# Kernel optimization log

Measured on AMD Instinct MI355X. Metric: run time of the kernel, lower is better.

Reference implementation:

```python
import jax, jax.numpy as jnp
import numpy as np

TEMPERATURE = 0.07
TAU_THRESHOLD = 0.5

B, D, K = 32768, 512, 2048


def _l2_normalize(x, axis=-1, eps=1e-12):
    # matches torch F.normalize: x / max(||x||, eps)
    n = jnp.linalg.norm(x, axis=axis, keepdims=True)
    return x / jnp.maximum(n, eps)


def setup_inputs() -> dict:
    key = jax.random.key(0)
    k1, k2, k3, k4 = jax.random.split(key, 4)
    embeddings = jax.random.normal(k1, (B, D), dtype=jnp.float32)
    best_similarity = jax.random.uniform(k2, (B,), dtype=jnp.float32)
    global_prototypes = jax.random.normal(k3, (K, D), dtype=jnp.float32)
    prototype_confidence = jax.random.uniform(k4, (K,), dtype=jnp.float32)
    return {
        "embeddings": embeddings,
        "best_similarity": best_similarity,
        "global_prototypes": global_prototypes,
        "prototype_confidence": prototype_confidence,
    }


def reference(embeddings, best_similarity, global_prototypes, prototype_confidence):
    en = _l2_normalize(embeddings, axis=1)          # [B, D]
    pn = _l2_normalize(global_prototypes, axis=1)   # [K, D]
    sims = jnp.einsum("bd,kd->bk", en, pn)          # [B, K] cosine sims
    best_proto_idx = jnp.argmax(sims, axis=1)       # [B]

    logits = sims / TEMPERATURE
    log_probs = jax.nn.log_softmax(logits, axis=1)  # [B, K]
    probs = jnp.exp(log_probs)
    entropy = -jnp.sum(probs * log_probs, axis=1)   # [B]
    max_entropy = jnp.log(jnp.float32(K))
    entropy_norm = entropy / (max_entropy + 1e-8)
    tau_adaptive = TAU_THRESHOLD - 0.2 * entropy_norm

    # confidence_weighted gating
    batch_conf = prototype_confidence[best_proto_idx]                     # [B]
    sigmoid_gate = jax.nn.sigmoid((best_similarity - tau_adaptive) / TEMPERATURE)
    gate = batch_conf * sigmoid_gate                                      # [B]

    target_protos = pn[best_proto_idx]                                    # [B, D]
    dist = jnp.linalg.norm(en - target_protos, axis=1)                    # [B]
    L_proto = jnp.mean(gate * dist)
    return (L_proto, gate)
```

## Files before the change

### kernel.cpp

```cpp
#include <hip/hip_runtime.h>
#include <math.h>


#define NB 32768
#define ND 512
#define NK 2048
#define TEMPR 0.07f
#define INV_T 14.285714285714286f
#define DX 5.0e-3f

typedef unsigned short u16;
typedef unsigned long long u64;
using bf16x8 = __attribute__((ext_vector_type(8))) short;
using u16x8 = __attribute__((ext_vector_type(8))) unsigned short;
using f32x16 = __attribute__((ext_vector_type(16))) float;

__device__ inline u16 bf_hi(float x) {
  unsigned u = __float_as_uint(x);
  u = u + 0x7FFFu + ((u >> 16) & 1u);
  return (u16)(u >> 16);
}
__device__ inline float bf_tof(u16 h) {
  return __uint_as_float(((unsigned)h) << 16);
}
__device__ inline void gload_lds16(const void* g, void* l) {
  __builtin_amdgcn_global_load_lds((const __attribute__((address_space(1))) void*)g,
                                   (__attribute__((address_space(3))) void*)l, 16, 0, 0);
}
#define MF(a, b, c) __builtin_amdgcn_mfma_f32_32x32x16_bf16((a), (b), (c), 0, 0, 0)

#define WAIT_LGKM0 { asm volatile("s_waitcnt lgkmcnt(0)" ::: "memory"); \
                     __builtin_amdgcn_sched_barrier(0); }
#define WAIT_VM6   { asm volatile("s_waitcnt vmcnt(6)" ::: "memory"); \
                     __builtin_amdgcn_sched_barrier(0); }
#define SBAR       { __builtin_amdgcn_s_barrier(); \
                     __builtin_amdgcn_sched_barrier(0); }

__global__ __launch_bounds__(256) void kprep_all(
    const float* __restrict__ P, const float* __restrict__ E,
    u16* __restrict__ Phi, float* __restrict__ invp,
    u16* __restrict__ Ehi, u16* __restrict__ Elo, int* __restrict__ cnt) {
  const int lane = threadIdx.x & 63, w = threadIdx.x >> 6;
  if (blockIdx.x < 512) {
    if (blockIdx.x == 0 && threadIdx.x == 0) *cnt = 0;
    const int p = blockIdx.x * 4 + w;
    const float4* pr = (const float4*)(P + (size_t)p * ND);
    float4 a = pr[2 * lane], b = pr[2 * lane + 1];
    float ss = a.x * a.x + a.y * a.y + a.z * a.z + a.w * a.w
             + b.x * b.x + b.y * b.y + b.z * b.z + b.w * b.w;
#pragma unroll
    for (int off = 32; off > 0; off >>= 1) ss += __shfl_xor(ss, off);
    const float inv = 1.0f / fmaxf(sqrtf(ss), 1e-12f);
    if (lane == 0) invp[p] = inv;
    u16x8 h8;
    h8[0] = bf_hi(a.x * inv); h8[1] = bf_hi(a.y * inv);
    h8[2] = bf_hi(a.z * inv); h8[3] = bf_hi(a.w * inv);
    h8[4] = bf_hi(b.x * inv); h8[5] = bf_hi(b.y * inv);
    h8[6] = bf_hi(b.z * inv); h8[7] = bf_hi(b.w * inv);
    const int kt = p >> 8, pl = p & 255;
    const size_t idx =
        ((size_t)((kt * 16 + (lane >> 2)) * 4 + (lane & 3)) * 256 + pl) * 8;
    *(u16x8*)(Phi + idx) = h8;
  } else {
    const int row = (blockIdx.x - 512) * 4 + w;
    const float4* er = (const float4*)(E + (size_t)row * ND);
    float4 a = er[lane], b = er[lane + 64];
    float ss = a.x * a.x + a.y * a.y + a.z * a.z + a.w * a.w
             + b.x * b.x + b.y * b.y + b.z * b.z + b.w * b.w;
#pragma unroll
    for (int off = 32; off > 0; off >>= 1) ss += __shfl_xor(ss, off);
    const float inv = 1.0f / fmaxf(sqrtf(ss), 1e-12f);
    ushort4 h4, l4;
#define PCNV4(dst_h, dst_l, f) { float n_ = (f) * inv; u16 hb_ = bf_hi(n_); \
  dst_h = hb_; dst_l = bf_hi(n_ - bf_tof(hb_)); }
    PCNV4(h4.x, l4.x, a.x) PCNV4(h4.y, l4.y, a.y)
    PCNV4(h4.z, l4.z, a.z) PCNV4(h4.w, l4.w, a.w)
    *(ushort4*)(Ehi + (size_t)row * ND + lane * 4) = h4;
    *(ushort4*)(Elo + (size_t)row * ND + lane * 4) = l4;
    PCNV4(h4.x, l4.x, b.x) PCNV4(h4.y, l4.y, b.y)
    PCNV4(h4.z, l4.z, b.z) PCNV4(h4.w, l4.w, b.w)
    *(ushort4*)(Ehi + (size_t)row * ND + (lane + 64) * 4) = h4;
    *(ushort4*)(Elo + (size_t)row * ND + (lane + 64) * 4) = l4;
#undef PCNV4
  }
}

#define UPD2(r, vv, pp) { \
  float x_ = fmaf((vv), INV_T, -INV_T); \
  float e_ = __expf(x_); \
  sS[r] += e_; uS[r] = fmaf(x_, e_, uS[r]); \
  bool u1_ = x_ > m1[r]; \
  float lo_ = u1_ ? m1[r] : x_; \
  m2[r] = fmaxf(m2[r], lo_); \
  m1[r] = u1_ ? x_ : m1[r]; \
  ix[r] = u1_ ? (pp) : ix[r]; }

__global__ __launch_bounds__(256, 2) void kmain_v11(
    const float* __restrict__ BS,
    const u16* __restrict__ PhiG,
    const u16* __restrict__ EhiG, const u16* __restrict__ EloG,
    const float* __restrict__ CONF,
    float* __restrict__ tau_ws, float* __restrict__ gd, float* __restrict__ gate_out,
    int* __restrict__ cnt, int* __restrict__ flags, u64* __restrict__ pk) {
  __shared__ u16 Ahi[2][2048], Alo[2][2048];
  __shared__ u16 Bhi[2][8192];

  const int t = threadIdx.x;
  const int lane = t & 63;
  const int w = t >> 6, wr = w >> 1, wc = w & 1;
  const int c = lane & 31, h = lane >> 5;
  const int swz = (blockIdx.x & 7) * 64 + (blockIdx.x >> 3);
  const int row0 = swz * 64;

  const u16* EhiA = EhiG + (size_t)(row0 + lane) * ND + w * 8;
  const u16* EloA = EloG + (size_t)(row0 + lane) * ND + w * 8;

  int boff[4];
#pragma unroll
  for (int i = 0; i < 4; ++i) boff[i] = (w * 256 + i * 64 + lane) * 8;

  const int ao0 = ((h)*64 + wr * 32 + c) * 8;
  const int ao1 = ((2 + h) * 64 + wr * 32 + c) * 8;
  const int bo0 = ((h)*256 + wc * 128 + c) * 8;
  const int bo1 = ((2 + h) * 256 + wc * 128 + c) * 8;

  f32x16 acc0, acc1, acc2, acc3;
#pragma unroll
  for (int i = 0; i < 16; ++i) { acc0[i] = 0.f; acc1[i] = 0.f; acc2[i] = 0.f; acc3[i] = 0.f; }
  float sS[16], uS[16], m1[16], m2[16];
  int ix[16];
#pragma unroll
  for (int r = 0; r < 16; ++r) {
    sS[r] = 0.f; uS[r] = 0.f; m1[r] = -3.0e38f; m2[r] = -3.0e38f; ix[r] = 0;
  }

#define SB11(tile_u16, nx) { \
  _Pragma("unroll") \
  for (int i = 0; i < 4; ++i) { \
    gload_lds16(PhiG + (tile_u16) + boff[i], &Bhi[nx][boff[i]]); \
  } }
#define SA11(col, nx) { \
  gload_lds16(EhiA + (col), &Ahi[nx][t * 8]); \
  gload_lds16(EloA + (col), &Alo[nx][t * 8]); }

  SB11(0, 0);
  SA11(0, 0);
  SB11(8192, 1);
  SA11(32, 1);
  WAIT_VM6;
  SBAR;

#pragma unroll 2
  for (int step = 0; step < 128; ++step) {
    const int cur = step & 1;
    const bf16x8 eh0 = *(const bf16x8*)&Ahi[cur][ao0];
    const bf16x8 el0 = *(const bf16x8*)&Alo[cur][ao0];
    const bf16x8 eh1 = *(const bf16x8*)&Ahi[cur][ao1];
    const bf16x8 el1 = *(const bf16x8*)&Alo[cur][ao1];
    const bf16x8 bh00 = *(const bf16x8*)&Bhi[cur][bo0];
    const bf16x8 bh01 = *(const bf16x8*)&Bhi[cur][bo0 + 256];
    const bf16x8 bh02 = *(const bf16x8*)&Bhi[cur][bo0 + 512];
    const bf16x8 bh03 = *(const bf16x8*)&Bhi[cur][bo0 + 768];
    const bf16x8 bh10 = *(const bf16x8*)&Bhi[cur][bo1];
    const bf16x8 bh11 = *(const bf16x8*)&Bhi[cur][bo1 + 256];
    const bf16x8 bh12 = *(const bf16x8*)&Bhi[cur][bo1 + 512];
    const bf16x8 bh13 = *(const bf16x8*)&Bhi[cur][bo1 + 768];

    acc0 = MF(eh0, bh00, acc0); acc1 = MF(eh0, bh01, acc1);
    acc2 = MF(eh0, bh02, acc2); acc3 = MF(eh0, bh03, acc3);
    acc0 = MF(el0, bh00, acc0); acc1 = MF(el0, bh01, acc1);
    acc2 = MF(el0, bh02, acc2); acc3 = MF(el0, bh03, acc3);

    WAIT_LGKM0;
    SBAR;

    const int ns = (step < 126) ? step + 2 : 127;
    SB11(ns * 8192, cur);
    SA11((ns & 15) * 32, cur);

    acc0 = MF(eh1, bh10, acc0); acc1 = MF(eh1, bh11, acc1);
    acc2 = MF(eh1, bh12, acc2); acc3 = MF(eh1, bh13, acc3);
    acc0 = MF(el1, bh10, acc0); acc1 = MF(el1, bh11, acc1);
    acc2 = MF(el1, bh12, acc2); acc3 = MF(el1, bh13, acc3);

    if ((step & 15) == 15) {
      const int pidb = (step >> 4) * 256 + wc * 128 + c;
#pragma unroll
      for (int r = 0; r < 16; ++r) {
        UPD2(r, acc0[r], pidb)
        UPD2(r, acc1[r], pidb + 32)
        UPD2(r, acc2[r], pidb + 64)
        UPD2(r, acc3[r], pidb + 96)
        acc0[r] = 0.f; acc1[r] = 0.f; acc2[r] = 0.f; acc3[r] = 0.f;
      }
    }

    WAIT_VM6;
    SBAR;
  }

  __syncthreads();

#pragma unroll
  for (int off = 1; off < 32; off <<= 1) {
#pragma unroll
    for (int r = 0; r < 16; ++r) {
      float m1o = __shfl_xor(m1[r], off);
      float m2o = __shfl_xor(m2[r], off);
      float so = __shfl_xor(sS[r], off);
      float uo = __shfl_xor(uS[r], off);
      int io = __shfl_xor(ix[r], off);
      sS[r] += so; uS[r] += uo;
      bool up = (m1o > m1[r]) || (m1o == m1[r] && io < ix[r]);
      float losr = (m1o > m1[r]) ? m1[r] : m1o;
      m2[r] = fmaxf(fmaxf(m2[r], m2o), losr);
      m1[r] = fmaxf(m1[r], m1o);
      ix[r] = up ? io : ix[r];
    }
  }

  float* mg = (float*)&Ahi[0][0];
  if (c == 0) {
#pragma unroll
    for (int r = 0; r < 16; ++r) {
      int rowl = (r & 3) + 8 * (r >> 2) + 4 * h;
      int base = ((wr * 2 + wc) * 32 + rowl) * 6;
      mg[base + 0] = m1[r];
      mg[base + 1] = sS[r];
      mg[base + 2] = uS[r];
      mg[base + 3] = __int_as_float(ix[r]);
      mg[base + 4] = m2[r];
    }
  }
  __syncthreads();

  if ((w & 1) == 0 && lane < 32) {
    const int rowl = lane;
    const int b0 = ((wr * 2 + 0) * 32 + rowl) * 6;
    const int b1 = ((wr * 2 + 1) * 32 + rowl) * 6;
    float m1a = mg[b0], s0 = mg[b0 + 1], u0 = mg[b0 + 2];
    int i0 = __float_as_int(mg[b0 + 3]);
    float m2a = mg[b0 + 4];
    float m1b = mg[b1], s1 = mg[b1 + 1], u1 = mg[b1 + 2];
    int i1 = __float_as_int(mg[b1 + 3]);
    float m2b = mg[b1 + 4];

    bool up = (m1b > m1a) || (m1b == m1a && i1 < i0);
    float m = fmaxf(m1a, m1b);
    float m2f = fmaxf(fmaxf(m2a, m2b), fminf(m1a, m1b));
    int idx = up ? i1 : i0;
    bool flg = (m - m2f) < DX;
    float s = s0 + s1, u = u0 + u1;

    float ent = logf(s) - u / s;
    float tau = 0.5f - 0.2f * (ent * (1.0f / (7.6246190071f + 1e-8f)));
    float simmax = fmaf(m, TEMPR, 1.0f);
    float dist = sqrtf(fmaxf(2.0f - 2.0f * simmax, 0.0f));
    int grow = row0 + wr * 32 + rowl;
    float g = CONF[idx] / (1.0f + __expf(-(BS[grow] - tau) * INV_T));
    gate_out[grow] = g;
    gd[grow] = g * dist;
    tau_ws[grow] = tau;
    if (flg) {
      pk[grow] = 0ull;
      int p = atomicAdd(cnt, 1);
      flags[p] = grow;
    }
  }
}

__global__ __launch_bounds__(256) void krescore4(
    const float* __restrict__ E, const float* __restrict__ P,
    const float* __restrict__ invp, const int* __restrict__ cnt,
    const int* __restrict__ flags, u64* __restrict__ pk) {
  const int n = *cnt;
  const int total = n * 16;
  const int t = threadIdx.x;
  const int k = t & 15;
  const int G = t >> 4;

  for (int ch = blockIdx.x; ch < total; ch += gridDim.x) {
    const int j = ch >> 4, q = ch & 15;
    const int row = flags[j];
    float4 e[8];
    float ss = 0.f;
    const float4* er = (const float4*)(E + (size_t)row * ND);
#pragma unroll
    for (int i = 0; i < 8; ++i) {
      e[i] = er[k + 16 * i];
      ss += e[i].x * e[i].x + e[i].y * e[i].y + e[i].z * e[i].z + e[i].w * e[i].w;
    }
#pragma unroll
    for (int o = 1; o < 16; o <<= 1) ss += __shfl_xor(ss, o);
    const float inv = 1.0f / fmaxf(sqrtf(ss), 1e-12f);
#pragma unroll
    for (int i = 0; i < 8; ++i) {
      e[i].x *= inv; e[i].y *= inv; e[i].z *= inv; e[i].w *= inv;
    }

    float best = -3.0e38f;
    int bidx = NK;
#pragma unroll 2
    for (int m = 0; m < 8; ++m) {
      const int p = q * 128 + G + 16 * m;
      const float4* pr = (const float4*)(P + (size_t)p * ND);
      float dot = 0.f;
#pragma unroll
      for (int i = 0; i < 8; ++i) {
        float4 a = pr[k + 16 * i];
        dot = fmaf(a.x, e[i].x, dot); dot = fmaf(a.y, e[i].y, dot);
        dot = fmaf(a.z, e[i].z, dot); dot = fmaf(a.w, e[i].w, dot);
      }
#pragma unroll
      for (int o = 1; o < 16; o <<= 1) dot += __shfl_xor(dot, o);
      float sim = dot * invp[p];
      if (sim > best) { best = sim; bidx = p; }
    }
    if (k == 0) {
      unsigned u = __float_as_uint(best);
      unsigned ord = (u & 0x80000000u) ? ~u : (u | 0x80000000u);
      u64 v = ((u64)ord << 32) | (unsigned)(NK - bidx);
      atomicMax(pk + row, v);
    }
  }
}

__global__ __launch_bounds__(1024) void kreduce2(
    float* __restrict__ gd, const float* __restrict__ BS,
    const float* __restrict__ CONF, const float* __restrict__ tau_ws,
    const int* __restrict__ cnt, const int* __restrict__ flags,
    const u64* __restrict__ pk, float* __restrict__ out0,
    float* __restrict__ gate_out) {
  __shared__ float red[1024];
  const int t = threadIdx.x;

  const int n = *cnt;
  for (int j = t; j < n; j += 1024) {
    const int row = flags[j];
    const u64 v = pk[row];
    const unsigned hi = (unsigned)(v >> 32);
    const int idx = NK - (int)(v & 0xFFFFFFFFu);
    const float sim = (hi & 0x80000000u) ? __uint_as_float(hi & 0x7FFFFFFFu)
                                         : __uint_as_float(~hi);
    const float tau = tau_ws[row];
    const float dist = sqrtf(fmaxf(2.0f - 2.0f * sim, 0.0f));
    const float g = CONF[idx] / (1.0f + __expf(-(BS[row] - tau) * INV_T));
    gate_out[row] = g;
    gd[row] = g * dist;
  }
  __syncthreads();

  float s = 0.f;
  const float4* g4 = (const float4*)gd;
  for (int i = t; i < 8192; i += 1024) {
    float4 v = g4[i];
    s += (v.x + v.y) + (v.z + v.w);
  }
  red[t] = s;
  __syncthreads();
  for (int off = 512; off > 0; off >>= 1) {
    if (t < off) red[t] += red[t + off];
    __syncthreads();
  }
  if (t == 0) out0[0] = red[0] * (1.0f / 32768.0f);
}

extern "C" void kernel_launch(void* const* d_in, const int* in_sizes, int n_in,
                              void* d_out, int out_size, void* d_ws, size_t ws_size,
                              hipStream_t stream) {
  const float* E = (const float*)d_in[0];
  const float* BS = (const float*)d_in[1];
  const float* P = (const float*)d_in[2];
  const float* CONF = (const float*)d_in[3];
  float* out = (float*)d_out;

  char* wsb = (char*)d_ws;
  u16* Phi = (u16*)wsb;
  u16* Ehi = (u16*)(wsb + ((size_t)4 << 20));
  u16* Elo = (u16*)(wsb + ((size_t)36 << 20));
  char* tail = wsb + ((size_t)68 << 20);
  float* tau_ws = (float*)tail;
  float* gd = (float*)(tail + 131072);
  int* flags = (int*)(tail + 2 * 131072);
  int* cnt = (int*)(tail + 3 * 131072);
  float* invp = (float*)(tail + 3 * 131072 + 4096);
  u64* pk = (u64*)(tail + 3 * 131072 + 4096 + 8192);

  kprep_all<<<8704, 256, 0, stream>>>(P, E, Phi, invp, Ehi, Elo, cnt);
  kmain_v11<<<512, 256, 0, stream>>>(BS, Phi, Ehi, Elo, CONF, tau_ws, gd,
                                     out + 1, cnt, flags, pk);
  krescore4<<<2048, 256, 0, stream>>>(E, P, invp, cnt, flags, pk);
  kreduce2<<<1, 1024, 0, stream>>>(gd, BS, CONF, tau_ws, cnt, flags, pk,
                                   out, out + 1);
}
```

Baseline: 317.8 us.

## Precompute embedding inverse norms and split rescore into finer prototype chunks

The prep kernel now stores each embedding row's inverse norm, so the rescore kernel no longer recomputes the norm with a shuffle reduction. Rescore work is split into 64 chunks of 32 prototypes per flagged row instead of 16 chunks of 128, on a grid four times larger, to spread the exact fp32 recheck across more blocks. The ambiguity threshold DX is tightened so fewer rows get flagged for rescoring. The cost is that the embedding row is reloaded four times as often per flagged row, and a tighter threshold risks missing true argmax ties if the bf16 error bound is not respected.

```diff
diff --git a/kernel.cpp b/kernel.cpp
--- a/kernel.cpp
+++ b/kernel.cpp
@@ -7,7 +7,7 @@
 #define NK 2048
 #define TEMPR 0.07f
 #define INV_T 14.285714285714286f
-#define DX 5.0e-3f
+#define DX 4.0e-3f
 
 typedef unsigned short u16;
 typedef unsigned long long u64;
@@ -39,7 +39,8 @@
 __global__ __launch_bounds__(256) void kprep_all(
     const float* __restrict__ P, const float* __restrict__ E,
     u16* __restrict__ Phi, float* __restrict__ invp,
-    u16* __restrict__ Ehi, u16* __restrict__ Elo, int* __restrict__ cnt) {
+    u16* __restrict__ Ehi, u16* __restrict__ Elo, float* __restrict__ inv_e,
+    int* __restrict__ cnt) {
   const int lane = threadIdx.x & 63, w = threadIdx.x >> 6;
   if (blockIdx.x < 512) {
     if (blockIdx.x == 0 && threadIdx.x == 0) *cnt = 0;
@@ -70,6 +71,7 @@
 #pragma unroll
     for (int off = 32; off > 0; off >>= 1) ss += __shfl_xor(ss, off);
     const float inv = 1.0f / fmaxf(sqrtf(ss), 1e-12f);
+    if (lane == 0) inv_e[row] = inv;
     ushort4 h4, l4;
 #define PCNV4(dst_h, dst_l, f) { float n_ = (f) * inv; u16 hb_ = bf_hi(n_); \
   dst_h = hb_; dst_l = bf_hi(n_ - bf_tof(hb_)); }
@@ -269,40 +271,31 @@
   }
 }
 
-__global__ __launch_bounds__(256) void krescore4(
+__global__ __launch_bounds__(256) void krescore5(
     const float* __restrict__ E, const float* __restrict__ P,
-    const float* __restrict__ invp, const int* __restrict__ cnt,
-    const int* __restrict__ flags, u64* __restrict__ pk) {
+    const float* __restrict__ invp, const float* __restrict__ inv_e,
+    const int* __restrict__ cnt, const int* __restrict__ flags,
+    u64* __restrict__ pk) {
   const int n = *cnt;
-  const int total = n * 16;
+  const int total = n * 64;
   const int t = threadIdx.x;
   const int k = t & 15;
   const int G = t >> 4;
 
   for (int ch = blockIdx.x; ch < total; ch += gridDim.x) {
-    const int j = ch >> 4, q = ch & 15;
+    const int j = ch >> 6, q = ch & 63;
     const int row = flags[j];
+    const float inve = inv_e[row];
     float4 e[8];
-    float ss = 0.f;
     const float4* er = (const float4*)(E + (size_t)row * ND);
 #pragma unroll
-    for (int i = 0; i < 8; ++i) {
-      e[i] = er[k + 16 * i];
-      ss += e[i].x * e[i].x + e[i].y * e[i].y + e[i].z * e[i].z + e[i].w * e[i].w;
-    }
-#pragma unroll
-    for (int o = 1; o < 16; o <<= 1) ss += __shfl_xor(ss, o);
-    const float inv = 1.0f / fmaxf(sqrtf(ss), 1e-12f);
-#pragma unroll
-    for (int i = 0; i < 8; ++i) {
-      e[i].x *= inv; e[i].y *= inv; e[i].z *= inv; e[i].w *= inv;
-    }
+    for (int i = 0; i < 8; ++i) e[i] = er[k + 16 * i];
 
     float best = -3.0e38f;
     int bidx = NK;
-#pragma unroll 2
-    for (int m = 0; m < 8; ++m) {
-      const int p = q * 128 + G + 16 * m;
+#pragma unroll
+    for (int m = 0; m < 2; ++m) {
+      const int p = q * 32 + G * 2 + m;
       const float4* pr = (const float4*)(P + (size_t)p * ND);
       float dot = 0.f;
 #pragma unroll
@@ -313,7 +306,7 @@
       }
 #pragma unroll
       for (int o = 1; o < 16; o <<= 1) dot += __shfl_xor(dot, o);
-      float sim = dot * invp[p];
+      float sim = dot * inve * invp[p];
       if (sim > best) { best = sim; bidx = p; }
     }
     if (k == 0) {
@@ -376,6 +369,7 @@
 
   char* wsb = (char*)d_ws;
   u16* Phi = (u16*)wsb;
+  float* inv_e = (float*)(wsb + ((size_t)2 << 20));
   u16* Ehi = (u16*)(wsb + ((size_t)4 << 20));
   u16* Elo = (u16*)(wsb + ((size_t)36 << 20));
   char* tail = wsb + ((size_t)68 << 20);
@@ -386,10 +380,10 @@
   float* invp = (float*)(tail + 3 * 131072 + 4096);
   u64* pk = (u64*)(tail + 3 * 131072 + 4096 + 8192);
 
-  kprep_all<<<8704, 256, 0, stream>>>(P, E, Phi, invp, Ehi, Elo, cnt);
+  kprep_all<<<8704, 256, 0, stream>>>(P, E, Phi, invp, Ehi, Elo, inv_e, cnt);
   kmain_v11<<<512, 256, 0, stream>>>(BS, Phi, Ehi, Elo, CONF, tau_ws, gd,
                                      out + 1, cnt, flags, pk);
-  krescore4<<<2048, 256, 0, stream>>>(E, P, invp, cnt, flags, pk);
+  krescore5<<<8192, 256, 0, stream>>>(E, P, invp, inv_e, cnt, flags, pk);
   kreduce2<<<1, 1024, 0, stream>>>(gd, BS, CONF, tau_ws, cnt, flags, pk,
                                    out, out + 1);
 }
```

Measured after the change: 335.7 us. 1.06x slower.
